# Performance work log

Measured on AMD Instinct MI355X. Metric: run time of the kernel, lower is better.

## Reference

```python
import jax, jax.numpy as jnp
import numpy as np

HEAD_DIM = 128
N_HEADS = 64
N_KV = 8
N_REP = 8
DIM = 5120
HID = 25600
EPS_LN = 1e-5
EPS_QK = 1e-6
MAX_SEQ = 1024
BSZ = 32


def rmsnorm(x, w, eps):
    xf = x.astype(jnp.float32)
    n = xf * jax.lax.rsqrt(jnp.mean(xf * xf, axis=-1, keepdims=True) + eps)
    return n.astype(x.dtype) * w


def rope(x, cos, sin):
    # x: [b, s, h, d]; cos/sin: [s, d//2]. Complex rotation on (even, odd) pairs.
    xr = x[..., 0::2]
    xi = x[..., 1::2]
    c = cos[None, :, None, :]
    s = sin[None, :, None, :]
    o_r = xr * c - xi * s
    o_i = xr * s + xi * c
    return jnp.stack([o_r, o_i], axis=-1).reshape(x.shape)


def setup_inputs() -> dict:
    key = jax.random.key(0)
    ks = jax.random.split(key, 12)
    seqlen = 1
    start_pos = MAX_SEQ - seqlen
    x = jax.random.normal(ks[0], (BSZ, seqlen, DIM), jnp.float32)
    pos = np.arange(start_pos, start_pos + seqlen)
    inv = 1.0 / (10000.0 ** (np.arange(0, HEAD_DIM, 2, dtype=np.float64) / HEAD_DIM))
    ang = pos[:, None] * inv[None, :]
    freqs_cos = jnp.asarray(np.cos(ang), jnp.float32)
    freqs_sin = jnp.asarray(np.sin(ang), jnp.float32)
    mask = jnp.zeros((1, 1, seqlen, start_pos + seqlen), jnp.float32)
    cache_k = jax.random.normal(ks[1], (BSZ, MAX_SEQ, N_KV, HEAD_DIM), jnp.float32)
    cache_v = jax.random.normal(ks[2], (BSZ, MAX_SEQ, N_KV, HEAD_DIM), jnp.float32)
    s = 0.02
    wq = jax.random.normal(ks[3], (N_HEADS * HEAD_DIM, DIM), jnp.float32) * s
    wk = jax.random.normal(ks[4], (N_KV * HEAD_DIM, DIM), jnp.float32) * s
    wv = jax.random.normal(ks[5], (N_KV * HEAD_DIM, DIM), jnp.float32) * s
    wo = jax.random.normal(ks[6], (DIM, N_HEADS * HEAD_DIM), jnp.float32) * s
    w1 = jax.random.normal(ks[7], (HID, DIM), jnp.float32) * s
    w2 = jax.random.normal(ks[8], (DIM, HID), jnp.float32) * s
    w3 = jax.random.normal(ks[9], (HID, DIM), jnp.float32) * s
    attn_norm_w = jnp.ones((DIM,), jnp.float32)
    ffn_norm_w = jnp.ones((DIM,), jnp.float32)
    q_norm_w = jnp.ones((HEAD_DIM,), jnp.float32)
    k_norm_w = jnp.ones((HEAD_DIM,), jnp.float32)
    return dict(x=x, start_pos=start_pos, freqs_cos=freqs_cos, freqs_sin=freqs_sin,
                mask=mask, cache_k=cache_k, cache_v=cache_v,
                wq=wq, wk=wk, wv=wv, wo=wo, w1=w1, w2=w2, w3=w3,
                attn_norm_w=attn_norm_w, ffn_norm_w=ffn_norm_w,
                q_norm_w=q_norm_w, k_norm_w=k_norm_w)


def reference(x, start_pos, freqs_cos, freqs_sin, mask, cache_k, cache_v,
              wq, wk, wv, wo, w1, w2, w3,
              attn_norm_w, ffn_norm_w, q_norm_w, k_norm_w):
    bsz, seqlen, _ = x.shape
    # --- attention branch ---
    an = rmsnorm(x, attn_norm_w, EPS_LN)
    xq = (an @ wq.T).reshape(bsz, seqlen, N_HEADS, HEAD_DIM)
    xk = (an @ wk.T).reshape(bsz, seqlen, N_KV, HEAD_DIM)
    xv = (an @ wv.T).reshape(bsz, seqlen, N_KV, HEAD_DIM)
    xq = rmsnorm(xq, q_norm_w, EPS_QK)
    xk = rmsnorm(xk, k_norm_w, EPS_QK)
    xq = rope(xq, freqs_cos, freqs_sin)
    xk = rope(xk, freqs_cos, freqs_sin)
    # KV-cache write (start_pos is a static Python int)
    cache_k = cache_k.at[:bsz, start_pos:start_pos + seqlen].set(xk)
    cache_v = cache_v.at[:bsz, start_pos:start_pos + seqlen].set(xv)
    L = start_pos + seqlen
    keys = cache_k[:bsz, :L]      # [b, L, g, d]
    values = cache_v[:bsz, :L]    # [b, L, g, d]
    # GQA via grouped einsum (math-equivalent to repeat_kv then matmul)
    qg = xq.reshape(bsz, seqlen, N_KV, N_REP, HEAD_DIM)  # head = g*N_REP + r
    scores = jnp.einsum('bqgrd,blgd->bgrql', qg, keys) / np.sqrt(HEAD_DIM).astype(np.float32)
    scores = scores + mask[:, :, None, :, :]  # [1,1,1,q,L] broadcast
    probs = jax.nn.softmax(scores.astype(jnp.float32), axis=-1).astype(xq.dtype)
    attn = jnp.einsum('bgrql,blgd->bqgrd', probs, values)
    attn = attn.reshape(bsz, seqlen, N_HEADS * HEAD_DIM)
    h = x + attn @ wo.T
    # --- SwiGLU FFN branch ---
    fn = rmsnorm(h, ffn_norm_w, EPS_LN)
    ff = (jax.nn.silu(fn @ w1.T) * (fn @ w3.T)) @ w2.T
    return h + ff
```

## Files before the change

kernel.cpp:

```cpp
#include <hip/hip_runtime.h>
#include <math.h>

#define DIM   5120
#define QD    8192
#define KVD   1024
#define NQKV  10240
#define NH    64
#define NKV   8
#define HD    128
#define HID   25600
#define SEQL  1024
#define BSZ   32
#define NSEG  4

typedef __attribute__((ext_vector_type(8))) short short8;
typedef __attribute__((ext_vector_type(4))) float f32x4;
typedef __attribute__((ext_vector_type(4))) unsigned short us4;

__device__ __forceinline__ unsigned short f2bf(float f) {
  unsigned u = __builtin_bit_cast(unsigned, f);
  unsigned r = u + 0x7fffu + ((u >> 16) & 1u);
  return (unsigned short)(r >> 16);
}
__device__ __forceinline__ float bf2f(unsigned short b) {
  return __builtin_bit_cast(float, (unsigned)b << 16);
}
__device__ __forceinline__ float fma4(float4 a, float4 b, float acc) {
  acc = fmaf(a.x, b.x, acc);
  acc = fmaf(a.y, b.y, acc);
  acc = fmaf(a.z, b.z, acc);
  acc = fmaf(a.w, b.w, acc);
  return acc;
}

__global__ __launch_bounds__(256) void rmsnorm_bf_kernel(
    const float* __restrict__ x, const float* __restrict__ w,
    unsigned short* __restrict__ out, float eps) {
  int b = blockIdx.x, t = threadIdx.x;
  const float4* xp = reinterpret_cast<const float4*>(x + (size_t)b * DIM);
  const float4* wp = reinterpret_cast<const float4*>(w);
  us4* op = reinterpret_cast<us4*>(out + (size_t)b * DIM);
  float4 v[5];
  float ss = 0.f;
#pragma unroll
  for (int j = 0; j < 5; ++j) {
    v[j] = xp[t + j * 256];
    ss = fma4(v[j], v[j], ss);
  }
#pragma unroll
  for (int m = 1; m < 64; m <<= 1) ss += __shfl_xor(ss, m);
  __shared__ float red[4];
  if ((t & 63) == 0) red[t >> 6] = ss;
  __syncthreads();
  float sc = rsqrtf((red[0] + red[1] + red[2] + red[3]) * (1.f / DIM) + eps);
#pragma unroll
  for (int j = 0; j < 5; ++j) {
    float4 wv = wp[t + j * 256];
    us4 o;
    o[0] = f2bf(v[j].x * sc * wv.x);
    o[1] = f2bf(v[j].y * sc * wv.y);
    o[2] = f2bf(v[j].z * sc * wv.z);
    o[3] = f2bf(v[j].w * sc * wv.w);
    op[t + j * 256] = o;
  }
}

template <int OUT_BF>
__device__ __forceinline__ void gemm_body(
    const unsigned short* __restrict__ Abf, const float* __restrict__ W,
    void* __restrict__ outp, int K, int k0, int kLen,
    int n0row, int n0col, int Nstride, int t) {
  int wid = t >> 6, lane = t & 63;
  int r = lane & 15, kg = lane >> 4;
  const float* wp = W + (size_t)(n0row + wid * 16 + r) * K + k0 + kg * 8;
  const unsigned short* ap0 = Abf + (size_t)r * K + k0 + kg * 8;
  const unsigned short* ap1 = ap0 + (size_t)16 * K;
  f32x4 acc0 = {0.f, 0.f, 0.f, 0.f}, acc1 = {0.f, 0.f, 0.f, 0.f};
#pragma unroll 2
  for (int kk = 0; kk < kLen; kk += 32) {
    float4 w0 = *reinterpret_cast<const float4*>(wp);
    float4 w1 = *reinterpret_cast<const float4*>(wp + 4);
    short8 wf;
    wf[0] = (short)f2bf(w0.x); wf[1] = (short)f2bf(w0.y);
    wf[2] = (short)f2bf(w0.z); wf[3] = (short)f2bf(w0.w);
    wf[4] = (short)f2bf(w1.x); wf[5] = (short)f2bf(w1.y);
    wf[6] = (short)f2bf(w1.z); wf[7] = (short)f2bf(w1.w);
    short8 a0 = *reinterpret_cast<const short8*>(ap0);
    short8 a1 = *reinterpret_cast<const short8*>(ap1);
    acc0 = __builtin_amdgcn_mfma_f32_16x16x32_bf16(wf, a0, acc0, 0, 0, 0);
    acc1 = __builtin_amdgcn_mfma_f32_16x16x32_bf16(wf, a1, acc1, 0, 0, 0);
    wp += 32; ap0 += 32; ap1 += 32;
  }
  int ncol = n0col + wid * 16 + kg * 4;
#pragma unroll
  for (int j = 0; j < 4; ++j) {
    if (OUT_BF) {
      unsigned short* o = (unsigned short*)outp;
      o[(size_t)r * Nstride + ncol + j] = f2bf(acc0[j]);
      o[(size_t)(r + 16) * Nstride + ncol + j] = f2bf(acc1[j]);
    } else {
      float* o = (float*)outp;
      o[(size_t)r * Nstride + ncol + j] = acc0[j];
      o[(size_t)(r + 16) * Nstride + ncol + j] = acc1[j];
    }
  }
}

__global__ __launch_bounds__(128) void qkv_gemm_kernel(
    const unsigned short* __restrict__ an_bf, const float* __restrict__ wq,
    const float* __restrict__ wk, const float* __restrict__ wv,
    float* __restrict__ part) {
  int n = blockIdx.x * 32;
  const float* W;
  int n0row;
  if (n < QD)            { W = wq; n0row = n; }
  else if (n < QD + KVD) { W = wk; n0row = n - QD; }
  else                   { W = wv; n0row = n - QD - KVD; }
  float* outp = part + (size_t)blockIdx.y * BSZ * NQKV;
  gemm_body<0>(an_bf, W, outp, DIM, blockIdx.y * 1280, 1280, n0row, n, NQKV,
               threadIdx.x);
}

__global__ __launch_bounds__(128) void wo_gemm_kernel(
    const unsigned short* __restrict__ ao_bf, const float* __restrict__ wo,
    float* __restrict__ part) {
  int n = blockIdx.x * 32;
  float* outp = part + (size_t)blockIdx.y * BSZ * DIM;
  gemm_body<0>(ao_bf, wo, outp, QD, blockIdx.y * 1024, 1024, n, n, DIM,
               threadIdx.x);
}

__global__ __launch_bounds__(128) void w13_gemm_kernel(
    const unsigned short* __restrict__ fn_bf, const float* __restrict__ w1,
    const float* __restrict__ w3, unsigned short* __restrict__ g13) {
  int n = blockIdx.x * 32;
  const float* W;
  int n0row;
  if (n < HID) { W = w1; n0row = n; }
  else         { W = w3; n0row = n - HID; }
  gemm_body<1>(fn_bf, W, g13, DIM, 0, DIM, n0row, n, 2 * HID, threadIdx.x);
}

__global__ __launch_bounds__(128) void w2_gemm_kernel(
    const unsigned short* __restrict__ gg_bf, const float* __restrict__ w2,
    float* __restrict__ part) {
  int n = blockIdx.x * 32;
  float* outp = part + (size_t)blockIdx.y * BSZ * DIM;
  gemm_body<0>(gg_bf, w2, outp, HID, blockIdx.y * 3200, 3200, n, n, DIM,
               threadIdx.x);
}

template <int SEGS, int OUT_BF>
__global__ __launch_bounds__(256) void combine_kernel(
    const float* __restrict__ part, const float* __restrict__ resid,
    void* __restrict__ out, int total) {
  int i = blockIdx.x * 256 + threadIdx.x;
  if (i >= total) return;
  float s = 0.f;
#pragma unroll
  for (int g = 0; g < SEGS; ++g) s += part[(size_t)g * total + i];
  if (resid) s += resid[i];
  if (OUT_BF) ((unsigned short*)out)[i] = f2bf(s);
  else        ((float*)out)[i] = s;
}

__global__ __launch_bounds__(64) void qknorm_rope_kernel(
    float* __restrict__ xqkv, const float* __restrict__ qw,
    const float* __restrict__ kw, const float* __restrict__ fcos,
    const float* __restrict__ fsin) {
  int h = blockIdx.x, b = blockIdx.y, j = threadIdx.x;
  float* p;
  const float* w;
  if (h < NH) { p = xqkv + (size_t)b * NQKV + h * HD; w = qw; }
  else        { p = xqkv + (size_t)b * NQKV + QD + (h - NH) * HD; w = kw; }
  float x0 = p[2 * j], x1 = p[2 * j + 1];
  float ss = x0 * x0 + x1 * x1;
#pragma unroll
  for (int m = 1; m < 64; m <<= 1) ss += __shfl_xor(ss, m);
  float sc = rsqrtf(ss * (1.f / HD) + 1e-6f);
  float n0 = x0 * sc * w[2 * j];
  float n1 = x1 * sc * w[2 * j + 1];
  float c = fcos[j], s = fsin[j];
  p[2 * j]     = n0 * c - n1 * s;
  p[2 * j + 1] = n0 * s + n1 * c;
}

__global__ __launch_bounds__(256) void attn_kernel(
    const float* __restrict__ xqkv, const float* __restrict__ ck,
    const float* __restrict__ cv, float* __restrict__ pacc,
    float* __restrict__ pml) {
  int g = blockIdx.x, b = blockIdx.y, z = blockIdx.z, t = threadIdx.x;
  __shared__ float qs[8][128];
  __shared__ float tk[128][33];
  __shared__ float tv[32][132];
  __shared__ float st[8][32];
  __shared__ float m_s[8], sum_s[8], fac_s[8];
  const float* qbase = xqkv + (size_t)b * NQKV;
  for (int i = t; i < 8 * 128; i += 256)
    qs[i >> 7][i & 127] = qbase[(g * 8 + (i >> 7)) * HD + (i & 127)];
  if (t < 8) { m_s[t] = -1e30f; sum_s[t] = 0.f; }
  int r = t >> 5, d5 = t & 31;
  float4 acc = make_float4(0.f, 0.f, 0.f, 0.f);
  for (int ti = 0; ti < 8; ++ti) {
    int l0 = z * 256 + ti * 32;
    __syncthreads();
#pragma unroll
    for (int jj = 0; jj < 4; ++jj) {
      int i = t + jj * 256;
      int l = i >> 5, d4 = i & 31;
      int gl = l0 + l;
      float4 kv, vv;
      if (gl == 1023) {
        kv = *reinterpret_cast<const float4*>(qbase + QD + g * HD + d4 * 4);
        vv = *reinterpret_cast<const float4*>(qbase + QD + KVD + g * HD + d4 * 4);
      } else {
        size_t base = (((size_t)b * SEQL + gl) * NKV + g) * HD + d4 * 4;
        kv = *reinterpret_cast<const float4*>(ck + base);
        vv = *reinterpret_cast<const float4*>(cv + base);
      }
      tk[d4 * 4 + 0][l] = kv.x;
      tk[d4 * 4 + 1][l] = kv.y;
      tk[d4 * 4 + 2][l] = kv.z;
      tk[d4 * 4 + 3][l] = kv.w;
      *reinterpret_cast<float4*>(&tv[l][d4 * 4]) = vv;
    }
    __syncthreads();
    {
      int l = t & 31, rr = t >> 5;
      float s = 0.f;
#pragma unroll 8
      for (int d = 0; d < 128; ++d) s = fmaf(qs[rr][d], tk[d][l], s);
      st[rr][l] = s * 0.08838834764831845f;
    }
    __syncthreads();
    {
      float sv = st[r][d5];
      float tm = sv;
#pragma unroll
      for (int m = 1; m < 32; m <<= 1) tm = fmaxf(tm, __shfl_xor(tm, m));
      float mo = m_s[r];
      float mn = fmaxf(mo, tm);
      float fac = __expf(mo - mn);
      float e = __expf(sv - mn);
      st[r][d5] = e;
      float ps = e;
#pragma unroll
      for (int m = 1; m < 32; m <<= 1) ps += __shfl_xor(ps, m);
      if (d5 == 0) {
        sum_s[r] = sum_s[r] * fac + ps;
        m_s[r] = mn;
        fac_s[r] = fac;
      }
    }
    __syncthreads();
    {
      float fac = fac_s[r];
      acc.x *= fac; acc.y *= fac; acc.z *= fac; acc.w *= fac;
#pragma unroll 4
      for (int l = 0; l < 32; ++l) {
        float p = st[r][l];
        float4 vv = *reinterpret_cast<const float4*>(&tv[l][d5 * 4]);
        acc.x = fmaf(p, vv.x, acc.x);
        acc.y = fmaf(p, vv.y, acc.y);
        acc.z = fmaf(p, vv.z, acc.z);
        acc.w = fmaf(p, vv.w, acc.w);
      }
    }
  }
  size_t idx = ((size_t)b * NH + g * 8 + r) * NSEG + z;
  *reinterpret_cast<float4*>(pacc + idx * HD + d5 * 4) = acc;
  if (d5 == 0) {
    pml[idx * 2]     = m_s[r];
    pml[idx * 2 + 1] = sum_s[r];
  }
}

__global__ __launch_bounds__(128) void attn_combine_kernel(
    const float* __restrict__ pacc, const float* __restrict__ pml,
    unsigned short* __restrict__ ao_bf) {
  int h = blockIdx.x, b = blockIdx.y, d = threadIdx.x;
  size_t base = ((size_t)b * NH + h) * NSEG;
  float M = -1e30f;
#pragma unroll
  for (int s = 0; s < NSEG; ++s) M = fmaxf(M, pml[(base + s) * 2]);
  float L = 0.f, o = 0.f;
#pragma unroll
  for (int s = 0; s < NSEG; ++s) {
    float w = __expf(pml[(base + s) * 2] - M);
    L += pml[(base + s) * 2 + 1] * w;
    o += pacc[(base + s) * HD + d] * w;
  }
  ao_bf[((size_t)b * NH + h) * HD + d] = f2bf(o / L);
}

__global__ __launch_bounds__(256) void silu_mul_bf_kernel(
    const unsigned short* __restrict__ g13, unsigned short* __restrict__ gg) {
  int j = blockIdx.x * 256 + threadIdx.x;
  int b = blockIdx.y;
  float a = bf2f(g13[(size_t)b * 2 * HID + j]);
  float c = bf2f(g13[(size_t)b * 2 * HID + HID + j]);
  gg[(size_t)b * HID + j] = f2bf((a / (1.f + __expf(-a))) * c);
}

extern "C" void kernel_launch(void* const* d_in, const int* in_sizes, int n_in,
                              void* d_out, int out_size, void* d_ws, size_t ws_size,
                              hipStream_t stream) {
  const float* x    = (const float*)d_in[0];
  const float* fcos = (const float*)d_in[2];
  const float* fsin = (const float*)d_in[3];
  const float* ck   = (const float*)d_in[5];
  const float* cv   = (const float*)d_in[6];
  const float* wq   = (const float*)d_in[7];
  const float* wk   = (const float*)d_in[8];
  const float* wv   = (const float*)d_in[9];
  const float* wo   = (const float*)d_in[10];
  const float* w1   = (const float*)d_in[11];
  const float* w2   = (const float*)d_in[12];
  const float* w3   = (const float*)d_in[13];
  const float* anw  = (const float*)d_in[14];
  const float* fnw  = (const float*)d_in[15];
  const float* qnw  = (const float*)d_in[16];
  const float* knw  = (const float*)d_in[17];
  float* out = (float*)d_out;

  char* wsb = (char*)d_ws;
  unsigned short* an_bf = (unsigned short*)wsb; wsb += (size_t)BSZ * DIM * 2;
  unsigned short* fn_bf = (unsigned short*)wsb; wsb += (size_t)BSZ * DIM * 2;
  unsigned short* ao_bf = (unsigned short*)wsb; wsb += (size_t)BSZ * QD * 2;
  unsigned short* gg_bf = (unsigned short*)wsb; wsb += (size_t)BSZ * HID * 2;
  unsigned short* g13_bf = (unsigned short*)wsb; wsb += (size_t)BSZ * 2 * HID * 2;
  float* xqkv = (float*)wsb; wsb += (size_t)BSZ * NQKV * 4;
  float* h    = (float*)wsb; wsb += (size_t)BSZ * DIM * 4;
  float* scratch = (float*)wsb;
  float* pacc = scratch;
  float* pml  = scratch + (size_t)BSZ * NH * NSEG * HD;

  rmsnorm_bf_kernel<<<BSZ, 256, 0, stream>>>(x, anw, an_bf, 1e-5f);
  qkv_gemm_kernel<<<dim3(NQKV / 32, 4), 128, 0, stream>>>(an_bf, wq, wk, wv, scratch);
  combine_kernel<4, 0><<<(BSZ * NQKV + 255) / 256, 256, 0, stream>>>(
      scratch, nullptr, xqkv, BSZ * NQKV);
  qknorm_rope_kernel<<<dim3(NH + NKV, BSZ), 64, 0, stream>>>(xqkv, qnw, knw, fcos, fsin);
  attn_kernel<<<dim3(NKV, BSZ, NSEG), 256, 0, stream>>>(xqkv, ck, cv, pacc, pml);
  attn_combine_kernel<<<dim3(NH, BSZ), 128, 0, stream>>>(pacc, pml, ao_bf);
  wo_gemm_kernel<<<dim3(DIM / 32, 8), 128, 0, stream>>>(ao_bf, wo, scratch);
  combine_kernel<8, 0><<<(BSZ * DIM + 255) / 256, 256, 0, stream>>>(
      scratch, x, h, BSZ * DIM);
  rmsnorm_bf_kernel<<<BSZ, 256, 0, stream>>>(h, fnw, fn_bf, 1e-5f);
  w13_gemm_kernel<<<dim3(2 * HID / 32, 1), 128, 0, stream>>>(fn_bf, w1, w3, g13_bf);
  silu_mul_bf_kernel<<<dim3(HID / 256, BSZ), 256, 0, stream>>>(g13_bf, gg_bf);
  w2_gemm_kernel<<<dim3(DIM / 32, 8), 128, 0, stream>>>(gg_bf, w2, scratch);
  combine_kernel<8, 0><<<(BSZ * DIM + 255) / 256, 256, 0, stream>>>(
      scratch, h, out, BSZ * DIM);
}
```

Baseline: 616.9 us.

## Software-pipeline GEMM loads, split K into two streams, fuse combine kernels, pack workspace

The GEMM inner loop now prefetches the next iteration's weight and activation fragments and runs two independent K-halves with separate accumulators. It also uses the packed v_cvt_pk_bf16_f32 instruction for the fp32-to-bf16 weight conversion. The QKV partial-sum combine is fused with qk-norm and RoPE, and the wo combine is fused with the FFN rmsnorm, which removes several launches and intermediate round trips. Workspace buffers are aliased into shared regions, which shrinks the footprint but depends on lifetimes not overlapping. The extra live registers from prefetching and the second accumulator set may reduce occupancy.

```diff
diff --git a/kernel.cpp b/kernel.cpp
--- a/kernel.cpp
+++ b/kernel.cpp
@@ -25,6 +25,19 @@
 __device__ __forceinline__ float bf2f(unsigned short b) {
   return __builtin_bit_cast(float, (unsigned)b << 16);
 }
+__device__ __forceinline__ unsigned cvt2(float lo, float hi) {
+  unsigned r;
+  asm("v_cvt_pk_bf16_f32 %0, %1, %2" : "=v"(r) : "v"(lo), "v"(hi));
+  return r;
+}
+__device__ __forceinline__ short8 cvt8(float4 a, float4 b) {
+  union { unsigned u[4]; short8 s; } o;
+  o.u[0] = cvt2(a.x, a.y);
+  o.u[1] = cvt2(a.z, a.w);
+  o.u[2] = cvt2(b.x, b.y);
+  o.u[3] = cvt2(b.z, b.w);
+  return o.s;
+}
 __device__ __forceinline__ float fma4(float4 a, float4 b, float acc) {
   acc = fmaf(a.x, b.x, acc);
   acc = fmaf(a.y, b.y, acc);
@@ -70,38 +83,65 @@
     const unsigned short* __restrict__ Abf, const float* __restrict__ W,
     void* __restrict__ outp, int K, int k0, int kLen,
     int n0row, int n0col, int Nstride, int t) {
-  int wid = t >> 6, lane = t & 63;
-  int r = lane & 15, kg = lane >> 4;
-  const float* wp = W + (size_t)(n0row + wid * 16 + r) * K + k0 + kg * 8;
-  const unsigned short* ap0 = Abf + (size_t)r * K + k0 + kg * 8;
-  const unsigned short* ap1 = ap0 + (size_t)16 * K;
-  f32x4 acc0 = {0.f, 0.f, 0.f, 0.f}, acc1 = {0.f, 0.f, 0.f, 0.f};
-#pragma unroll 2
-  for (int kk = 0; kk < kLen; kk += 32) {
-    float4 w0 = *reinterpret_cast<const float4*>(wp);
-    float4 w1 = *reinterpret_cast<const float4*>(wp + 4);
-    short8 wf;
-    wf[0] = (short)f2bf(w0.x); wf[1] = (short)f2bf(w0.y);
-    wf[2] = (short)f2bf(w0.z); wf[3] = (short)f2bf(w0.w);
-    wf[4] = (short)f2bf(w1.x); wf[5] = (short)f2bf(w1.y);
-    wf[6] = (short)f2bf(w1.z); wf[7] = (short)f2bf(w1.w);
-    short8 a0 = *reinterpret_cast<const short8*>(ap0);
-    short8 a1 = *reinterpret_cast<const short8*>(ap1);
-    acc0 = __builtin_amdgcn_mfma_f32_16x16x32_bf16(wf, a0, acc0, 0, 0, 0);
-    acc1 = __builtin_amdgcn_mfma_f32_16x16x32_bf16(wf, a1, acc1, 0, 0, 0);
-    wp += 32; ap0 += 32; ap1 += 32;
+  const int wid = t >> 6, lane = t & 63;
+  const int r = lane & 15, kg = lane >> 4;
+  const int half = kLen >> 1;
+  const float* wpA = W + (size_t)(n0row + wid * 16 + r) * K + k0 + kg * 8;
+  const float* wpB = wpA + half;
+  const unsigned short* apA0 = Abf + (size_t)r * K + k0 + kg * 8;
+  const unsigned short* apA1 = apA0 + (size_t)16 * K;
+  const unsigned short* apB0 = apA0 + half;
+  const unsigned short* apB1 = apA1 + half;
+  f32x4 accA0 = {0.f, 0.f, 0.f, 0.f}, accA1 = accA0;
+  f32x4 accB0 = accA0, accB1 = accA0;
+  float4 wa0 = *reinterpret_cast<const float4*>(wpA);
+  float4 wa1 = *reinterpret_cast<const float4*>(wpA + 4);
+  float4 wb0 = *reinterpret_cast<const float4*>(wpB);
+  float4 wb1 = *reinterpret_cast<const float4*>(wpB + 4);
+  short8 aa0 = *reinterpret_cast<const short8*>(apA0);
+  short8 aa1 = *reinterpret_cast<const short8*>(apA1);
+  short8 ab0 = *reinterpret_cast<const short8*>(apB0);
+  short8 ab1 = *reinterpret_cast<const short8*>(apB1);
+  for (int kk = 0; kk < half - 32; kk += 32) {
+    wpA += 32; wpB += 32; apA0 += 32; apA1 += 32; apB0 += 32; apB1 += 32;
+    float4 nwa0 = *reinterpret_cast<const float4*>(wpA);
+    float4 nwa1 = *reinterpret_cast<const float4*>(wpA + 4);
+    float4 nwb0 = *reinterpret_cast<const float4*>(wpB);
+    float4 nwb1 = *reinterpret_cast<const float4*>(wpB + 4);
+    short8 naa0 = *reinterpret_cast<const short8*>(apA0);
+    short8 naa1 = *reinterpret_cast<const short8*>(apA1);
+    short8 nab0 = *reinterpret_cast<const short8*>(apB0);
+    short8 nab1 = *reinterpret_cast<const short8*>(apB1);
+    short8 wfa = cvt8(wa0, wa1);
+    short8 wfb = cvt8(wb0, wb1);
+    accA0 = __builtin_amdgcn_mfma_f32_16x16x32_bf16(wfa, aa0, accA0, 0, 0, 0);
+    accA1 = __builtin_amdgcn_mfma_f32_16x16x32_bf16(wfa, aa1, accA1, 0, 0, 0);
+    accB0 = __builtin_amdgcn_mfma_f32_16x16x32_bf16(wfb, ab0, accB0, 0, 0, 0);
+    accB1 = __builtin_amdgcn_mfma_f32_16x16x32_bf16(wfb, ab1, accB1, 0, 0, 0);
+    wa0 = nwa0; wa1 = nwa1; wb0 = nwb0; wb1 = nwb1;
+    aa0 = naa0; aa1 = naa1; ab0 = nab0; ab1 = nab1;
+  }
+  {
+    short8 wfa = cvt8(wa0, wa1);
+    short8 wfb = cvt8(wb0, wb1);
+    accA0 = __builtin_amdgcn_mfma_f32_16x16x32_bf16(wfa, aa0, accA0, 0, 0, 0);
+    accA1 = __builtin_amdgcn_mfma_f32_16x16x32_bf16(wfa, aa1, accA1, 0, 0, 0);
+    accB0 = __builtin_amdgcn_mfma_f32_16x16x32_bf16(wfb, ab0, accB0, 0, 0, 0);
+    accB1 = __builtin_amdgcn_mfma_f32_16x16x32_bf16(wfb, ab1, accB1, 0, 0, 0);
   }
   int ncol = n0col + wid * 16 + kg * 4;
 #pragma unroll
   for (int j = 0; j < 4; ++j) {
+    float v0 = accA0[j] + accB0[j];
+    float v1 = accA1[j] + accB1[j];
     if (OUT_BF) {
       unsigned short* o = (unsigned short*)outp;
-      o[(size_t)r * Nstride + ncol + j] = f2bf(acc0[j]);
-      o[(size_t)(r + 16) * Nstride + ncol + j] = f2bf(acc1[j]);
+      o[(size_t)r * Nstride + ncol + j] = f2bf(v0);
+      o[(size_t)(r + 16) * Nstride + ncol + j] = f2bf(v1);
     } else {
       float* o = (float*)outp;
-      o[(size_t)r * Nstride + ncol + j] = acc0[j];
-      o[(size_t)(r + 16) * Nstride + ncol + j] = acc1[j];
+      o[(size_t)r * Nstride + ncol + j] = v0;
+      o[(size_t)(r + 16) * Nstride + ncol + j] = v1;
     }
   }
 }
@@ -150,39 +190,95 @@
                threadIdx.x);
 }
 
-template <int SEGS, int OUT_BF>
+__global__ __launch_bounds__(64) void qkv_finish_kernel(
+    const float* __restrict__ part, const float* __restrict__ qw,
+    const float* __restrict__ kw, const float* __restrict__ fcos,
+    const float* __restrict__ fsin, float* __restrict__ xqkv) {
+  int h = blockIdx.x, b = blockIdx.y, j = threadIdx.x;
+  int base;
+  const float* w = nullptr;
+  int dorope = 1;
+  if (h < NH)            { base = h * HD; w = qw; }
+  else if (h < NH + NKV) { base = QD + (h - NH) * HD; w = kw; }
+  else                   { base = QD + KVD + (h - NH - NKV) * HD; dorope = 0; }
+  size_t off = (size_t)b * NQKV + base;
+  float s0 = 0.f, s1 = 0.f;
+#pragma unroll
+  for (int g = 0; g < 4; ++g) {
+    const float* p = part + (size_t)g * BSZ * NQKV + off;
+    s0 += p[2 * j];
+    s1 += p[2 * j + 1];
+  }
+  if (dorope) {
+    float ss = s0 * s0 + s1 * s1;
+#pragma unroll
+    for (int m = 1; m < 64; m <<= 1) ss += __shfl_xor(ss, m);
+    float sc = rsqrtf(ss * (1.f / HD) + 1e-6f);
+    float n0 = s0 * sc * w[2 * j];
+    float n1 = s1 * sc * w[2 * j + 1];
+    float c = fcos[j], s = fsin[j];
+    xqkv[off + 2 * j]     = n0 * c - n1 * s;
+    xqkv[off + 2 * j + 1] = n0 * s + n1 * c;
+  } else {
+    xqkv[off + 2 * j]     = s0;
+    xqkv[off + 2 * j + 1] = s1;
+  }
+}
+
+__global__ __launch_bounds__(256) void wo_finish_kernel(
+    const float* __restrict__ part, const float* __restrict__ x,
+    const float* __restrict__ fw, float* __restrict__ h,
+    unsigned short* __restrict__ fn_bf, float eps) {
+  int b = blockIdx.x, t = threadIdx.x;
+  const float4* xp = reinterpret_cast<const float4*>(x + (size_t)b * DIM);
+  const float4* wp = reinterpret_cast<const float4*>(fw);
+  float4* hp = reinterpret_cast<float4*>(h + (size_t)b * DIM);
+  us4* fp = reinterpret_cast<us4*>(fn_bf + (size_t)b * DIM);
+  float4 v[5];
+  float ss = 0.f;
+#pragma unroll
+  for (int j = 0; j < 5; ++j) {
+    int idx = t + j * 256;
+    float4 s = xp[idx];
+#pragma unroll
+    for (int g = 0; g < 8; ++g) {
+      float4 p = reinterpret_cast<const float4*>(
+          part + (size_t)g * BSZ * DIM + (size_t)b * DIM)[idx];
+      s.x += p.x; s.y += p.y; s.z += p.z; s.w += p.w;
+    }
+    v[j] = s;
+    ss = fma4(s, s, ss);
+    hp[idx] = s;
+  }
+#pragma unroll
+  for (int m = 1; m < 64; m <<= 1) ss += __shfl_xor(ss, m);
+  __shared__ float red[4];
+  if ((t & 63) == 0) red[t >> 6] = ss;
+  __syncthreads();
+  float sc = rsqrtf((red[0] + red[1] + red[2] + red[3]) * (1.f / DIM) + eps);
+#pragma unroll
+  for (int j = 0; j < 5; ++j) {
+    float4 wv = wp[t + j * 256];
+    us4 o;
+    o[0] = f2bf(v[j].x * sc * wv.x);
+    o[1] = f2bf(v[j].y * sc * wv.y);
+    o[2] = f2bf(v[j].z * sc * wv.z);
+    o[3] = f2bf(v[j].w * sc * wv.w);
+    fp[t + j * 256] = o;
+  }
+}
+
+template <int SEGS>
 __global__ __launch_bounds__(256) void combine_kernel(
     const float* __restrict__ part, const float* __restrict__ resid,
-    void* __restrict__ out, int total) {
+    float* __restrict__ out, int total) {
   int i = blockIdx.x * 256 + threadIdx.x;
   if (i >= total) return;
   float s = 0.f;
 #pragma unroll
   for (int g = 0; g < SEGS; ++g) s += part[(size_t)g * total + i];
   if (resid) s += resid[i];
-  if (OUT_BF) ((unsigned short*)out)[i] = f2bf(s);
-  else        ((float*)out)[i] = s;
-}
-
-__global__ __launch_bounds__(64) void qknorm_rope_kernel(
-    float* __restrict__ xqkv, const float* __restrict__ qw,
-    const float* __restrict__ kw, const float* __restrict__ fcos,
-    const float* __restrict__ fsin) {
-  int h = blockIdx.x, b = blockIdx.y, j = threadIdx.x;
-  float* p;
-  const float* w;
-  if (h < NH) { p = xqkv + (size_t)b * NQKV + h * HD; w = qw; }
-  else        { p = xqkv + (size_t)b * NQKV + QD + (h - NH) * HD; w = kw; }
-  float x0 = p[2 * j], x1 = p[2 * j + 1];
-  float ss = x0 * x0 + x1 * x1;
-#pragma unroll
-  for (int m = 1; m < 64; m <<= 1) ss += __shfl_xor(ss, m);
-  float sc = rsqrtf(ss * (1.f / HD) + 1e-6f);
-  float n0 = x0 * sc * w[2 * j];
-  float n1 = x1 * sc * w[2 * j + 1];
-  float c = fcos[j], s = fsin[j];
-  p[2 * j]     = n0 * c - n1 * s;
-  p[2 * j + 1] = n0 * s + n1 * c;
+  out[i] = s;
 }
 
 __global__ __launch_bounds__(256) void attn_kernel(
@@ -324,31 +420,32 @@
   float* out = (float*)d_out;
 
   char* wsb = (char*)d_ws;
-  unsigned short* an_bf = (unsigned short*)wsb; wsb += (size_t)BSZ * DIM * 2;
-  unsigned short* fn_bf = (unsigned short*)wsb; wsb += (size_t)BSZ * DIM * 2;
-  unsigned short* ao_bf = (unsigned short*)wsb; wsb += (size_t)BSZ * QD * 2;
-  unsigned short* gg_bf = (unsigned short*)wsb; wsb += (size_t)BSZ * HID * 2;
-  unsigned short* g13_bf = (unsigned short*)wsb; wsb += (size_t)BSZ * 2 * HID * 2;
-  float* xqkv = (float*)wsb; wsb += (size_t)BSZ * NQKV * 4;
-  float* h    = (float*)wsb; wsb += (size_t)BSZ * DIM * 4;
   float* scratch = (float*)wsb;
+  char* R1 = wsb + 5505024;
+  char* R2 = R1 + 3276800;
+  char* R3 = R2 + 1638400;
+  char* R4 = R3 + 655360;
+  unsigned short* an_bf  = (unsigned short*)R1;
+  unsigned short* ao_bf  = (unsigned short*)(R1 + 327680);
+  unsigned short* g13_bf = (unsigned short*)R1;
+  float*          xqkv   = (float*)R2;
+  unsigned short* gg_bf  = (unsigned short*)R2;
+  float*          h      = (float*)R3;
+  unsigned short* fn_bf  = (unsigned short*)R4;
   float* pacc = scratch;
   float* pml  = scratch + (size_t)BSZ * NH * NSEG * HD;
 
   rmsnorm_bf_kernel<<<BSZ, 256, 0, stream>>>(x, anw, an_bf, 1e-5f);
   qkv_gemm_kernel<<<dim3(NQKV / 32, 4), 128, 0, stream>>>(an_bf, wq, wk, wv, scratch);
-  combine_kernel<4, 0><<<(BSZ * NQKV + 255) / 256, 256, 0, stream>>>(
-      scratch, nullptr, xqkv, BSZ * NQKV);
-  qknorm_rope_kernel<<<dim3(NH + NKV, BSZ), 64, 0, stream>>>(xqkv, qnw, knw, fcos, fsin);
+  qkv_finish_kernel<<<dim3(NH + 2 * NKV, BSZ), 64, 0, stream>>>(
+      scratch, qnw, knw, fcos, fsin, xqkv);
   attn_kernel<<<dim3(NKV, BSZ, NSEG), 256, 0, stream>>>(xqkv, ck, cv, pacc, pml);
   attn_combine_kernel<<<dim3(NH, BSZ), 128, 0, stream>>>(pacc, pml, ao_bf);
   wo_gemm_kernel<<<dim3(DIM / 32, 8), 128, 0, stream>>>(ao_bf, wo, scratch);
-  combine_kernel<8, 0><<<(BSZ * DIM + 255) / 256, 256, 0, stream>>>(
-      scratch, x, h, BSZ * DIM);
-  rmsnorm_bf_kernel<<<BSZ, 256, 0, stream>>>(h, fnw, fn_bf, 1e-5f);
+  wo_finish_kernel<<<BSZ, 256, 0, stream>>>(scratch, x, fnw, h, fn_bf, 1e-5f);
   w13_gemm_kernel<<<dim3(2 * HID / 32, 1), 128, 0, stream>>>(fn_bf, w1, w3, g13_bf);
   silu_mul_bf_kernel<<<dim3(HID / 256, BSZ), 256, 0, stream>>>(g13_bf, gg_bf);
   w2_gemm_kernel<<<dim3(DIM / 32, 8), 128, 0, stream>>>(gg_bf, w2, scratch);
-  combine_kernel<8, 0><<<(BSZ * DIM + 255) / 256, 256, 0, stream>>>(
+  combine_kernel<8><<<(BSZ * DIM + 255) / 256, 256, 0, stream>>>(
       scratch, h, out, BSZ * DIM);
 }
```

Result: slower. 663.8 us (+7.6%).
